# Kernel optimization log

Hardware: AMD Instinct MI355X
Metric: run time of the kernel (lower is better)

The kernel has to match this reference:

```python
import jax, jax.numpy as jnp
import numpy as np

B, N, C, H = 8, 1024, 768, 12
D = C // H
SCALE = D ** -0.5


def setup_inputs() -> dict:
    key = jax.random.key(0)
    k1, k2, k3 = jax.random.split(key, 3)
    x = jax.random.normal(k1, (B, N, C), dtype=jnp.float32)
    w_qkv = jax.random.normal(k2, (C, 3 * C), dtype=jnp.float32) * (C ** -0.5)
    w_proj = jax.random.normal(k3, (C, C), dtype=jnp.float32) * (C ** -0.5)
    b_proj = jnp.zeros((C,), dtype=jnp.float32)
    return {"x": x, "w_qkv": w_qkv, "w_proj": w_proj, "b_proj": b_proj}


def reference(x, w_qkv, w_proj, b_proj):
    Bx, Nx, Cx = x.shape
    # qkv projection (no bias), split into q,k,v with shape [B, H, N, D]
    qkv = (x @ w_qkv).reshape(Bx, Nx, 3, H, D).transpose(2, 0, 3, 1, 4)
    q, k, v = qkv[0], qkv[1], qkv[2]
    # full attention matrix [B, H, N, N] (matches torch module's explicit materialization)
    attn = jnp.einsum('bhqd,bhkd->bhqk', q, k) * SCALE
    attn = jax.nn.softmax(attn, axis=-1)
    out = jnp.einsum('bhqk,bhkd->bhqd', attn, v)
    out = out.transpose(0, 2, 1, 3).reshape(Bx, Nx, Cx)
    return out @ w_proj + b_proj
```

## Files before the change

kernel.cpp:

```cpp
#include <hip/hip_runtime.h>


typedef unsigned short u16;
typedef short s16x8 __attribute__((ext_vector_type(8)));
typedef float f32x4 __attribute__((ext_vector_type(4)));
typedef u16   u16x8 __attribute__((ext_vector_type(8)));
typedef u16   u16x4 __attribute__((ext_vector_type(4)));

__device__ __forceinline__ u16 f2bf(float f) {
    unsigned int u = __builtin_bit_cast(unsigned int, f);
    u += 0x7FFFu + ((u >> 16) & 1u);
    return (u16)(u >> 16);
}

__device__ __forceinline__ void gload16(const u16* g, u16* l) {
    __builtin_amdgcn_global_load_lds(
        (const __attribute__((address_space(1))) unsigned int*)g,
        (__attribute__((address_space(3))) unsigned int*)l, 16, 0, 0);
}

__global__ __launch_bounds__(256) void prep(
    const float* __restrict__ x, u16* __restrict__ xb,
    const float* __restrict__ wq, u16* __restrict__ wqT,
    const float* __restrict__ wp, u16* __restrict__ wpT) {
    __shared__ float ts[32][33];
    const int g = blockIdx.x, tid = threadIdx.x;
    if (g < 3072) {
        const size_t i = ((size_t)g * 256 + tid) * 8;
        float4 v0 = *(const float4*)(x + i);
        float4 v1 = *(const float4*)(x + i + 4);
        u16x8 p;
        p[0] = f2bf(v0.x); p[1] = f2bf(v0.y); p[2] = f2bf(v0.z); p[3] = f2bf(v0.w);
        p[4] = f2bf(v1.x); p[5] = f2bf(v1.y); p[6] = f2bf(v1.z); p[7] = f2bf(v1.w);
        *(u16x8*)(xb + i) = p;
        return;
    }
    const float* in; u16* out; int K, Nc, n0, k0;
    if (g < 4800) {
        int gg = g - 3072; in = wq; out = wqT; K = 768; Nc = 2304;
        n0 = (gg % 72) * 32; k0 = (gg / 72) * 32;
    } else {
        int gg = g - 4800; in = wp; out = wpT; K = 768; Nc = 768;
        n0 = (gg % 24) * 32; k0 = (gg / 24) * 32;
    }
    const int tx = tid & 31, ty = tid >> 5;
#pragma unroll
    for (int j = 0; j < 4; ++j) {
        int r = ty + j * 8;
        ts[r][tx] = in[(size_t)(k0 + r) * Nc + n0 + tx];
    }
    __syncthreads();
#pragma unroll
    for (int j = 0; j < 4; ++j) {
        int r = ty + j * 8;
        out[(size_t)(n0 + r) * K + k0 + tx] = f2bf(ts[tx][r]);
    }
}

__global__ __launch_bounds__(256) void gemm_qkv(
    const u16* __restrict__ Aq, const u16* __restrict__ Bt,
    u16* __restrict__ qb, u16* __restrict__ kb, u16* __restrict__ vbT) {
    __shared__ __align__(16) u16 As[2][128 * 32];
    __shared__ __align__(16) u16 Bs[2][128 * 32];
    const int tid = threadIdx.x;
    const int lane = tid & 63, w = tid >> 6;
    const int m15 = lane & 15, quad = lane >> 4;
    const int wy = w >> 1, wx = w & 1;
    const int g = blockIdx.x;
    const int xcd = g & 7, s = g >> 3;
    const int yt = xcd * 8 + (s & 7), xt = s >> 3;
    const int m0 = yt * 128, n0 = xt * 128;
    const int srow16 = lane >> 2;
    const int scol = (lane & 3) * 8;

    f32x4 acc[4][4] = {};

    for (int k0 = 0; k0 < 768; k0 += 64) {
        __syncthreads();
#pragma unroll
        for (int j = 0; j < 2; ++j) {
            int rA = w * 32 + j * 16 + srow16;
            const u16* a0 = Aq + (size_t)(m0 + rA) * 768 + k0 + scol;
            const u16* b0 = Bt + (size_t)(n0 + rA) * 768 + k0 + scol;
            gload16(a0,      &As[0][(w * 32 + j * 16) * 32]);
            gload16(a0 + 32, &As[1][(w * 32 + j * 16) * 32]);
            gload16(b0,      &Bs[0][(w * 32 + j * 16) * 32]);
            gload16(b0 + 32, &Bs[1][(w * 32 + j * 16) * 32]);
        }
        __syncthreads();
#pragma unroll
        for (int h = 0; h < 2; ++h) {
            s16x8 av[4], bv[4];
#pragma unroll
            for (int ri = 0; ri < 4; ++ri)
                av[ri] = *(const s16x8*)&As[h][(wy * 64 + ri * 16 + m15) * 32 + quad * 8];
#pragma unroll
            for (int ci = 0; ci < 4; ++ci)
                bv[ci] = *(const s16x8*)&Bs[h][(wx * 64 + ci * 16 + m15) * 32 + quad * 8];
#pragma unroll
            for (int ri = 0; ri < 4; ++ri)
#pragma unroll
                for (int ci = 0; ci < 4; ++ci)
                    acc[ri][ci] = __builtin_amdgcn_mfma_f32_16x16x32_bf16(av[ri], bv[ci], acc[ri][ci], 0, 0, 0);
        }
    }

    const int which = xt / 6;
#pragma unroll
    for (int ri = 0; ri < 4; ++ri) {
        int mb = m0 + wy * 64 + ri * 16 + (quad << 2);
        int b = mb >> 10, row = mb & 1023;
#pragma unroll
        for (int ci = 0; ci < 4; ++ci) {
            int col = n0 + wx * 64 + ci * 16 + m15 - which * 768;
            int h = col >> 6, d = col & 63;
            size_t bhi = (size_t)(b * 12 + h);
            if (which == 2) {
                u16x4 pk;
#pragma unroll
                for (int rg = 0; rg < 4; ++rg) pk[rg] = f2bf(acc[ri][ci][rg]);
                *(u16x4*)&vbT[(bhi * 64 + d) * 1024 + row] = pk;
            } else {
                u16* dst = which ? kb : qb;
#pragma unroll
                for (int rg = 0; rg < 4; ++rg)
                    dst[(bhi * 1024 + row + rg) * 64 + d] = f2bf(acc[ri][ci][rg]);
            }
        }
    }
}

__global__ __launch_bounds__(256) void gemm_proj(
    const u16* __restrict__ A, const u16* __restrict__ Bt,
    const float* __restrict__ bias, float* __restrict__ out) {
    __shared__ __align__(16) u16 As[2][128 * 32];
    __shared__ __align__(16) u16 Bs[2][128 * 32];
    const int tid = threadIdx.x;
    const int lane = tid & 63, w = tid >> 6;
    const int m15 = lane & 15, quad = lane >> 4;
    const int wy = w >> 1, wx = w & 1;
    const int g = blockIdx.x;
    const int xcd = g & 7, s = g >> 3;
    const int yt = xcd * 8 + (s & 7), xt = s >> 3;
    const int m0 = yt * 128, n0 = xt * 128;
    const int srow16 = lane >> 2;
    const int scol = (lane & 3) * 8;

    f32x4 acc[4][4] = {};

    for (int k0 = 0; k0 < 768; k0 += 64) {
        __syncthreads();
#pragma unroll
        for (int j = 0; j < 2; ++j) {
            int rA = w * 32 + j * 16 + srow16;
            const u16* a0 = A  + (size_t)(m0 + rA) * 768 + k0 + scol;
            const u16* b0 = Bt + (size_t)(n0 + rA) * 768 + k0 + scol;
            gload16(a0,      &As[0][(w * 32 + j * 16) * 32]);
            gload16(a0 + 32, &As[1][(w * 32 + j * 16) * 32]);
            gload16(b0,      &Bs[0][(w * 32 + j * 16) * 32]);
            gload16(b0 + 32, &Bs[1][(w * 32 + j * 16) * 32]);
        }
        __syncthreads();
#pragma unroll
        for (int h = 0; h < 2; ++h) {
            s16x8 av[4], bv[4];
#pragma unroll
            for (int ri = 0; ri < 4; ++ri)
                av[ri] = *(const s16x8*)&As[h][(wy * 64 + ri * 16 + m15) * 32 + quad * 8];
#pragma unroll
            for (int ci = 0; ci < 4; ++ci)
                bv[ci] = *(const s16x8*)&Bs[h][(wx * 64 + ci * 16 + m15) * 32 + quad * 8];
#pragma unroll
            for (int ri = 0; ri < 4; ++ri)
#pragma unroll
                for (int ci = 0; ci < 4; ++ci)
                    acc[ri][ci] = __builtin_amdgcn_mfma_f32_16x16x32_bf16(av[ri], bv[ci], acc[ri][ci], 0, 0, 0);
        }
    }

#pragma unroll
    for (int ri = 0; ri < 4; ++ri) {
        int mb = m0 + wy * 64 + ri * 16 + (quad << 2);
#pragma unroll
        for (int ci = 0; ci < 4; ++ci) {
            int n = n0 + wx * 64 + ci * 16 + m15;
            float bv_ = bias[n];
#pragma unroll
            for (int rg = 0; rg < 4; ++rg)
                out[(size_t)(mb + rg) * 768 + n] = acc[ri][ci][rg] + bv_;
        }
    }
}

#define KS 72

__global__ __launch_bounds__(256) void attn_mfma(
    const u16* __restrict__ qb, const u16* __restrict__ kb,
    const u16* __restrict__ vbT, u16* __restrict__ aout) {
    __shared__ __align__(16) u16 Ks[64 * KS];
    __shared__ __align__(16) u16 Vs[64 * KS];
    __shared__ __align__(16) u16 Ps[4][16 * KS];
    const int tid = threadIdx.x, lane = tid & 63, w = tid >> 6;
    const int m15 = lane & 15, quad = lane >> 4;
    const int g = blockIdx.x;
    const int xcd = g & 7, s = g >> 3;
    const int bh = xcd * 12 + (s % 12);
    const int q0 = (s / 12) * 64;

    s16x8 aq[2];
    {
        const u16* qp = qb + ((size_t)bh * 1024 + q0 + w * 16 + m15) * 64 + quad * 8;
        aq[0] = *(const s16x8*)qp;
        aq[1] = *(const s16x8*)(qp + 32);
    }

    s16x8 bones;
#pragma unroll
    for (int j = 0; j < 8; ++j) bones[j] = (m15 == 0) ? (short)0x3F80 : (short)0;

    f32x4 oacc[4] = {};
    f32x4 lacc = {};

    const int srow = tid >> 2;
    const int soff = (tid & 3) * 16;
    const u16* kbase = kb + (size_t)bh * 1024 * 64;
    const u16* vbase = vbT + (size_t)bh * 64 * 1024;
    const float CE   = 0.125f * 1.44269504f;
    const float MOFF = 12.0f * 1.44269504f;

    for (int kt = 0; kt < 16; ++kt) {
        __syncthreads();
        const u16* kpp = kbase + ((size_t)kt * 64 + srow) * 64 + soff;
        const u16* vpp = vbase + (size_t)srow * 1024 + kt * 64 + soff;
        *(u16x8*)&Ks[srow * KS + soff]     = *(const u16x8*)kpp;
        *(u16x8*)&Ks[srow * KS + soff + 8] = *(const u16x8*)(kpp + 8);
        *(u16x8*)&Vs[srow * KS + soff]     = *(const u16x8*)vpp;
        *(u16x8*)&Vs[srow * KS + soff + 8] = *(const u16x8*)(vpp + 8);
        __syncthreads();

        f32x4 sacc[4] = {};
#pragma unroll
        for (int ci = 0; ci < 4; ++ci)
#pragma unroll
            for (int ch = 0; ch < 2; ++ch) {
                s16x8 bk = *(const s16x8*)&Ks[(ci * 16 + m15) * KS + quad * 8 + 32 * ch];
                sacc[ci] = __builtin_amdgcn_mfma_f32_16x16x32_bf16(aq[ch], bk, sacc[ci], 0, 0, 0);
            }

#pragma unroll
        for (int ci = 0; ci < 4; ++ci)
#pragma unroll
            for (int reg = 0; reg < 4; ++reg) {
                float pv = __builtin_amdgcn_exp2f(sacc[ci][reg] * CE - MOFF);
                unsigned int u = __builtin_bit_cast(unsigned int, pv);
                Ps[w][(quad * 4 + reg) * KS + ci * 16 + m15] = (u16)(u >> 16);
            }

        s16x8 ap[2];
        ap[0] = *(const s16x8*)&Ps[w][m15 * KS + quad * 8];
        ap[1] = *(const s16x8*)&Ps[w][m15 * KS + quad * 8 + 32];
#pragma unroll
        for (int ch = 0; ch < 2; ++ch)
            lacc = __builtin_amdgcn_mfma_f32_16x16x32_bf16(ap[ch], bones, lacc, 0, 0, 0);
#pragma unroll
        for (int di = 0; di < 4; ++di)
#pragma unroll
            for (int ch = 0; ch < 2; ++ch) {
                s16x8 bv = *(const s16x8*)&Vs[(di * 16 + m15) * KS + quad * 8 + 32 * ch];
                oacc[di] = __builtin_amdgcn_mfma_f32_16x16x32_bf16(ap[ch], bv, oacc[di], 0, 0, 0);
            }
    }

    float linv[4];
#pragma unroll
    for (int reg = 0; reg < 4; ++reg)
        linv[reg] = 1.0f / __shfl(lacc[reg], lane & 48);

    const int b = bh / 12, h = bh - b * 12;
#pragma unroll
    for (int di = 0; di < 4; ++di)
#pragma unroll
        for (int reg = 0; reg < 4; ++reg) {
            int q = q0 + w * 16 + quad * 4 + reg;
            aout[((size_t)b * 1024 + q) * 768 + h * 64 + di * 16 + m15] =
                f2bf(oacc[di][reg] * linv[reg]);
        }
}

extern "C" void kernel_launch(void* const* d_in, const int* in_sizes, int n_in,
                              void* d_out, int out_size, void* d_ws, size_t ws_size,
                              hipStream_t stream) {
    const float* x      = (const float*)d_in[0];
    const float* w_qkv  = (const float*)d_in[1];
    const float* w_proj = (const float*)d_in[2];
    const float* b_proj = (const float*)d_in[3];
    float* out = (float*)d_out;

    char* ws = (char*)d_ws;
    u16* wqkvT  = (u16*)ws;  ws += (size_t)2304 * 768 * 2;
    u16* wprojT = (u16*)ws;  ws += (size_t)768 * 768 * 2;
    u16* qb     = (u16*)ws;  ws += (size_t)96 * 1024 * 64 * 2;
    u16* kb     = (u16*)ws;  ws += (size_t)96 * 1024 * 64 * 2;
    u16* vbT    = (u16*)ws;  ws += (size_t)96 * 1024 * 64 * 2;
    u16* aout   = (u16*)ws;  ws += (size_t)8192 * 768 * 2;
    u16* xb     = aout;

    prep<<<dim3(5376), 256, 0, stream>>>(x, xb, w_qkv, wqkvT, w_proj, wprojT);
    gemm_qkv<<<dim3(1152), 256, 0, stream>>>(xb, wqkvT, qb, kb, vbT);
    attn_mfma<<<dim3(1536), 256, 0, stream>>>(qb, kb, vbT, aout);
    gemm_proj<<<dim3(384), 256, 0, stream>>>(aout, wprojT, b_proj, out);
}
```

Before: 204.4 us.

## Process two query sub-tiles per wave in attention to halve K/V staging

Each attention block now handles 128 query rows instead of 64, so each wave computes two 16-row query sub-tiles against the same K/V tiles held in LDS. This halves how often K and V are loaded into shared memory and gets more MFMA work from each LDS read. The score MFMA has its operands swapped (K as A, Q as B), which makes the P tile come out transposed so it can be stored as packed 4-wide vectors instead of scalar stores. In exchange, register pressure rises and the grid shrinks to 768 blocks, which may reduce occupancy.

```diff
diff --git a/kernel.cpp b/kernel.cpp
--- a/kernel.cpp
+++ b/kernel.cpp
@@ -199,27 +199,28 @@
     const u16* __restrict__ vbT, u16* __restrict__ aout) {
     __shared__ __align__(16) u16 Ks[64 * KS];
     __shared__ __align__(16) u16 Vs[64 * KS];
-    __shared__ __align__(16) u16 Ps[4][16 * KS];
+    __shared__ __align__(16) u16 Ps[8][16 * KS];
     const int tid = threadIdx.x, lane = tid & 63, w = tid >> 6;
     const int m15 = lane & 15, quad = lane >> 4;
     const int g = blockIdx.x;
     const int xcd = g & 7, s = g >> 3;
     const int bh = xcd * 12 + (s % 12);
-    const int q0 = (s / 12) * 64;
-
-    s16x8 aq[2];
-    {
-        const u16* qp = qb + ((size_t)bh * 1024 + q0 + w * 16 + m15) * 64 + quad * 8;
-        aq[0] = *(const s16x8*)qp;
-        aq[1] = *(const s16x8*)(qp + 32);
+    const int q0 = (s / 12) * 128;
+
+    s16x8 aq[2][2];
+#pragma unroll
+    for (int qs = 0; qs < 2; ++qs) {
+        const u16* qp = qb + ((size_t)bh * 1024 + q0 + w * 32 + qs * 16 + m15) * 64 + quad * 8;
+        aq[qs][0] = *(const s16x8*)qp;
+        aq[qs][1] = *(const s16x8*)(qp + 32);
     }
 
     s16x8 bones;
 #pragma unroll
     for (int j = 0; j < 8; ++j) bones[j] = (m15 == 0) ? (short)0x3F80 : (short)0;
 
-    f32x4 oacc[4] = {};
-    f32x4 lacc = {};
+    f32x4 oacc[2][4] = {};
+    f32x4 lacc[2] = {};
 
     const int srow = tid >> 2;
     const int soff = (tid & 3) * 16;
@@ -238,53 +239,65 @@
         *(u16x8*)&Vs[srow * KS + soff + 8] = *(const u16x8*)(vpp + 8);
         __syncthreads();
 
-        f32x4 sacc[4] = {};
-#pragma unroll
-        for (int ci = 0; ci < 4; ++ci)
+        f32x4 sacc[2][4] = {};
+#pragma unroll
+        for (int t = 0; t < 4; ++t)
 #pragma unroll
             for (int ch = 0; ch < 2; ++ch) {
-                s16x8 bk = *(const s16x8*)&Ks[(ci * 16 + m15) * KS + quad * 8 + 32 * ch];
-                sacc[ci] = __builtin_amdgcn_mfma_f32_16x16x32_bf16(aq[ch], bk, sacc[ci], 0, 0, 0);
-            }
-
-#pragma unroll
-        for (int ci = 0; ci < 4; ++ci)
-#pragma unroll
-            for (int reg = 0; reg < 4; ++reg) {
-                float pv = __builtin_amdgcn_exp2f(sacc[ci][reg] * CE - MOFF);
-                unsigned int u = __builtin_bit_cast(unsigned int, pv);
-                Ps[w][(quad * 4 + reg) * KS + ci * 16 + m15] = (u16)(u >> 16);
-            }
-
-        s16x8 ap[2];
-        ap[0] = *(const s16x8*)&Ps[w][m15 * KS + quad * 8];
-        ap[1] = *(const s16x8*)&Ps[w][m15 * KS + quad * 8 + 32];
-#pragma unroll
-        for (int ch = 0; ch < 2; ++ch)
-            lacc = __builtin_amdgcn_mfma_f32_16x16x32_bf16(ap[ch], bones, lacc, 0, 0, 0);
+                s16x8 ak = *(const s16x8*)&Ks[(t * 16 + m15) * KS + quad * 8 + 32 * ch];
+                sacc[0][t] = __builtin_amdgcn_mfma_f32_16x16x32_bf16(ak, aq[0][ch], sacc[0][t], 0, 0, 0);
+                sacc[1][t] = __builtin_amdgcn_mfma_f32_16x16x32_bf16(ak, aq[1][ch], sacc[1][t], 0, 0, 0);
+            }
+
+#pragma unroll
+        for (int qs = 0; qs < 2; ++qs)
+#pragma unroll
+            for (int t = 0; t < 4; ++t) {
+                u16x4 pk;
+#pragma unroll
+                for (int reg = 0; reg < 4; ++reg) {
+                    float pv = __builtin_amdgcn_exp2f(sacc[qs][t][reg] * CE - MOFF);
+                    unsigned int u = __builtin_bit_cast(unsigned int, pv);
+                    pk[reg] = (u16)(u >> 16);
+                }
+                *(u16x4*)&Ps[w * 2 + qs][m15 * KS + t * 16 + quad * 4] = pk;
+            }
+
+        s16x8 ap[2][2];
+#pragma unroll
+        for (int qs = 0; qs < 2; ++qs) {
+            ap[qs][0] = *(const s16x8*)&Ps[w * 2 + qs][m15 * KS + quad * 8];
+            ap[qs][1] = *(const s16x8*)&Ps[w * 2 + qs][m15 * KS + quad * 8 + 32];
+#pragma unroll
+            for (int ch = 0; ch < 2; ++ch)
+                lacc[qs] = __builtin_amdgcn_mfma_f32_16x16x32_bf16(ap[qs][ch], bones, lacc[qs], 0, 0, 0);
+        }
 #pragma unroll
         for (int di = 0; di < 4; ++di)
 #pragma unroll
             for (int ch = 0; ch < 2; ++ch) {
                 s16x8 bv = *(const s16x8*)&Vs[(di * 16 + m15) * KS + quad * 8 + 32 * ch];
-                oacc[di] = __builtin_amdgcn_mfma_f32_16x16x32_bf16(ap[ch], bv, oacc[di], 0, 0, 0);
-            }
-    }
-
-    float linv[4];
-#pragma unroll
-    for (int reg = 0; reg < 4; ++reg)
-        linv[reg] = 1.0f / __shfl(lacc[reg], lane & 48);
+                oacc[0][di] = __builtin_amdgcn_mfma_f32_16x16x32_bf16(ap[0][ch], bv, oacc[0][di], 0, 0, 0);
+                oacc[1][di] = __builtin_amdgcn_mfma_f32_16x16x32_bf16(ap[1][ch], bv, oacc[1][di], 0, 0, 0);
+            }
+    }
 
     const int b = bh / 12, h = bh - b * 12;
 #pragma unroll
-    for (int di = 0; di < 4; ++di)
-#pragma unroll
-        for (int reg = 0; reg < 4; ++reg) {
-            int q = q0 + w * 16 + quad * 4 + reg;
-            aout[((size_t)b * 1024 + q) * 768 + h * 64 + di * 16 + m15] =
-                f2bf(oacc[di][reg] * linv[reg]);
-        }
+    for (int qs = 0; qs < 2; ++qs) {
+        float linv[4];
+#pragma unroll
+        for (int reg = 0; reg < 4; ++reg)
+            linv[reg] = 1.0f / __shfl(lacc[qs][reg], lane & 48);
+#pragma unroll
+        for (int di = 0; di < 4; ++di)
+#pragma unroll
+            for (int reg = 0; reg < 4; ++reg) {
+                int q = q0 + w * 32 + qs * 16 + quad * 4 + reg;
+                aout[((size_t)b * 1024 + q) * 768 + h * 64 + di * 16 + m15] =
+                    f2bf(oacc[qs][di][reg] * linv[reg]);
+            }
+    }
 }
 
 extern "C" void kernel_launch(void* const* d_in, const int* in_sizes, int n_in,
@@ -307,6 +320,6 @@
 
     prep<<<dim3(5376), 256, 0, stream>>>(x, xb, w_qkv, wqkvT, w_proj, wprojT);
     gemm_qkv<<<dim3(1152), 256, 0, stream>>>(xb, wqkvT, qb, kb, vbT);
-    attn_mfma<<<dim3(1536), 256, 0, stream>>>(qb, kb, vbT, aout);
+    attn_mfma<<<dim3(768), 256, 0, stream>>>(qb, kb, vbT, aout);
     gemm_proj<<<dim3(384), 256, 0, stream>>>(aout, wprojT, b_proj, out);
 }
```

Result: faster. 187.1 us (-8.5%).
